# Optimization experiments

Measured on AMD Instinct MI355X. Metric: run time of the kernel, lower is better.

The kernel has to match this reference:

```python
import jax, jax.numpy as jnp
import numpy as np

B, L, E = 4, 1024, 1024
H = 16
HD = E // H
CLIP = 16
SCALE = 1.0 / np.sqrt(HD)


def setup_inputs() -> dict:
    key = jax.random.key(0)
    ks = jax.random.split(key, 13)
    def lin(k, fan_in, fan_out, gain):
        # xavier_uniform
        limit = gain * np.sqrt(6.0 / (fan_in + fan_out))
        return jax.random.uniform(k, (fan_out, fan_in), jnp.float32, -limit, limit)
    inv_sqrt2 = 1.0 / np.sqrt(2.0)
    return {
        "query": jax.random.normal(ks[0], (B, L, E), jnp.float32),
        "key": jax.random.normal(ks[1], (B, L, E), jnp.float32),
        "value": jax.random.normal(ks[2], (B, L, E), jnp.float32),
        "wq": lin(ks[3], E, E, inv_sqrt2), "bq": jnp.zeros((E,), jnp.float32),
        "wk": lin(ks[4], E, E, inv_sqrt2), "bk": jnp.zeros((E,), jnp.float32),
        "wv": lin(ks[5], E, E, inv_sqrt2), "bv": jnp.zeros((E,), jnp.float32),
        "wo": lin(ks[6], E, E, 1.0), "bo": jnp.zeros((E,), jnp.float32),
        "rel_k": jax.random.normal(ks[7], (2 * CLIP + 1, HD), jnp.float32) * 0.02,
        "rel_v": jax.random.normal(ks[8], (2 * CLIP + 1, HD), jnp.float32) * 0.02,
    }


def _heads(x):  # (B, L, E) -> (B, H, L, HD)
    return x.reshape(B, L, H, HD).transpose(0, 2, 1, 3)


def reference(query, key, value, wq, bq, wk, bk, wv, bv, wo, bo, rel_k, rel_v):
    q = _heads(query @ wq.T + bq)
    k = _heads(key @ wk.T + bk)
    v = _heads(value @ wv.T + bv)

    # relative-position index matrix (L_q, L_k), clipped to [-CLIP, CLIP]
    pos = jnp.arange(L)
    dist = jnp.clip(pos[None, :] - pos[:, None], -CLIP, CLIP) + CLIP
    r_k = rel_k[dist]  # (L, L, HD)
    r_v = rel_v[dist]  # (L, L, HD)

    dot = jnp.einsum('bhid,bhjd->bhij', q, k)
    rel = jnp.einsum('bhid,ijd->bhij', q, r_k)
    scores = (dot + rel) * SCALE
    attn = jax.nn.softmax(scores, axis=-1)

    y = jnp.einsum('bhij,bhjd->bhid', attn, v) + jnp.einsum('bhij,ijd->bhid', attn, r_v)
    y = y.transpose(0, 2, 1, 3).reshape(B, L, E)
    return y @ wo.T + bo
```

## Files before the change

kernel.cpp:

```cpp
#include <hip/hip_runtime.h>

#define BB 4
#define LL 1024
#define EE 1024
#define HH 16
#define HD 64
#define NBUCKET 33
#define SCALE 0.125f
#define SC2 (0.125f * 1.44269504088896f)

typedef unsigned short u16;
using f32x4 = __attribute__((ext_vector_type(4))) float;
using s16x8 = __attribute__((ext_vector_type(8))) short;

__device__ __forceinline__ u16 f2bf(float f) {
  union { float f; unsigned u; } x; x.f = f;
  unsigned r = (x.u + 0x7fffu + ((x.u >> 16) & 1u)) >> 16;
  return (u16)r;
}

__device__ __forceinline__ void gld_lds16(const void* g, void* s) {
  __builtin_amdgcn_global_load_lds((const __attribute__((address_space(1))) void*)g,
                                   (__attribute__((address_space(3))) void*)s, 16, 0, 0);
}

__device__ __forceinline__ float qsum16(float s) {
  s += __shfl_xor(s, 1); s += __shfl_xor(s, 2);
  s += __shfl_xor(s, 4); s += __shfl_xor(s, 8);
  return s;
}

__global__ __launch_bounds__(256) void cvt3_bf16(const float* __restrict__ a,
                                                 const float* __restrict__ b,
                                                 const float* __restrict__ c,
                                                 u16* __restrict__ oa, u16* __restrict__ ob,
                                                 u16* __restrict__ oc, int n4) {
  const int z = blockIdx.y;
  const float* in = z == 0 ? a : (z == 1 ? b : c);
  u16* out = z == 0 ? oa : (z == 1 ? ob : oc);
  int i = blockIdx.x * 256 + threadIdx.x;
  if (i < n4) {
    float4 f = ((const float4*)in)[i];
    ushort4 o;
    o.x = f2bf(f.x); o.y = f2bf(f.y); o.z = f2bf(f.z); o.w = f2bf(f.w);
    ((ushort4*)out)[i] = o;
  }
}

__global__ __launch_bounds__(256) void cvt4r_bf16(const float* __restrict__ a,
                                                  const float* __restrict__ b,
                                                  const float* __restrict__ c,
                                                  const float* __restrict__ d,
                                                  const float* __restrict__ rk,
                                                  u16* __restrict__ oa, u16* __restrict__ ob,
                                                  u16* __restrict__ oc, u16* __restrict__ od,
                                                  u16* __restrict__ ork, int n4) {
  const int z = blockIdx.z;
  int i = blockIdx.x * 256 + threadIdx.x;
  if (z == 4) {
    if (i < 48 * 64) ork[i] = (i < 33 * 64) ? f2bf(rk[i]) : (u16)0;
    return;
  }
  const float* in = z == 0 ? a : (z == 1 ? b : (z == 2 ? c : d));
  u16* out = z == 0 ? oa : (z == 1 ? ob : (z == 2 ? oc : od));
  if (i < n4) {
    float4 f = ((const float4*)in)[i];
    ushort4 o;
    o.x = f2bf(f.x); o.y = f2bf(f.y); o.z = f2bf(f.z); o.w = f2bf(f.w);
    ((ushort4*)out)[i] = o;
  }
}

template <int MODE>
__device__ __forceinline__ void gemm128_bt(const u16* __restrict__ A,
                                           const u16* __restrict__ Bw,
                                           const float* __restrict__ bias,
                                           u16* __restrict__ obf,
                                           float* __restrict__ ofp,
                                           int M, int N, int K, int m0, int n0) {
  __shared__ u16 a_sm[128 * 64];
  __shared__ u16 b_sm[128 * 64];
  const int tid = threadIdx.x;
  const int wave = tid >> 6, lane = tid & 63;
  const int row16 = lane & 15, quad = lane >> 4;
  const int wr = (wave >> 1) * 64, wc = (wave & 1) * 64;
  const int srow = lane >> 3, scol = (lane & 7) * 8;

  f32x4 acc[4][4] = {};

  for (int k0 = 0; k0 < K; k0 += 64) {
#pragma unroll
    for (int t = 0; t < 4; ++t) {
      const int chunk = wave * 4 + t;
      const int r = chunk * 8 + srow;
      gld_lds16(A + (size_t)(m0 + r) * K + k0 + scol, a_sm + chunk * 512);
      gld_lds16(Bw + (size_t)(n0 + r) * K + k0 + scol, b_sm + chunk * 512);
    }
    __syncthreads();
#pragma unroll
    for (int ks = 0; ks < 2; ++ks) {
      s16x8 af[4], bf[4];
#pragma unroll
      for (int mi = 0; mi < 4; ++mi)
        af[mi] = *(const s16x8*)&a_sm[(wr + mi * 16 + row16) * 64 + ks * 32 + quad * 8];
#pragma unroll
      for (int ni = 0; ni < 4; ++ni)
        bf[ni] = *(const s16x8*)&b_sm[(wc + ni * 16 + row16) * 64 + ks * 32 + quad * 8];
#pragma unroll
      for (int mi = 0; mi < 4; ++mi)
#pragma unroll
        for (int ni = 0; ni < 4; ++ni)
          acc[mi][ni] = __builtin_amdgcn_mfma_f32_16x16x32_bf16(af[mi], bf[ni], acc[mi][ni], 0, 0, 0);
    }
    __syncthreads();
  }

#pragma unroll
  for (int mi = 0; mi < 4; ++mi)
#pragma unroll
    for (int ni = 0; ni < 4; ++ni) {
      const int n = n0 + wc + ni * 16 + row16;
      const float bn = bias[n];
      if (MODE == 2) {
        const int mr0 = m0 + wr + mi * 16 + quad * 4;
        const int b = mr0 >> 10, l = mr0 & 1023;
        const int h = n >> 6, hd = n & 63;
        ushort4 o;
        o.x = f2bf(acc[mi][ni][0] + bn);
        o.y = f2bf(acc[mi][ni][1] + bn);
        o.z = f2bf(acc[mi][ni][2] + bn);
        o.w = f2bf(acc[mi][ni][3] + bn);
        *(ushort4*)&obf[((size_t)((b * HH + h) * HD + hd)) * LL + l] = o;
      } else {
#pragma unroll
        for (int r = 0; r < 4; ++r) {
          const int m = m0 + wr + mi * 16 + quad * 4 + r;
          const float v = acc[mi][ni][r] + bn;
          if (MODE == 0) {
            const int b = m >> 10, l = m & 1023, h = n >> 6, hd = n & 63;
            obf[((size_t)((b * HH + h) * LL + l)) * HD + hd] = f2bf(v);
          } else {
            ofp[(size_t)m * N + n] = v;
          }
        }
      }
    }
}

__global__ __launch_bounds__(256) void proj_gemm(
    const u16* __restrict__ xq, const u16* __restrict__ xk, const u16* __restrict__ xv,
    const u16* __restrict__ wqb, const u16* __restrict__ wkb, const u16* __restrict__ wvb,
    const float* __restrict__ bq, const float* __restrict__ bk, const float* __restrict__ bv,
    u16* __restrict__ oq, u16* __restrict__ ok, u16* __restrict__ ovt) {
  if (blockIdx.z == 0)
    gemm128_bt<0>(xq, wqb, bq, oq, nullptr, BB * LL, EE, EE, blockIdx.y * 128, blockIdx.x * 128);
  else if (blockIdx.z == 1)
    gemm128_bt<0>(xk, wkb, bk, ok, nullptr, BB * LL, EE, EE, blockIdx.y * 128, blockIdx.x * 128);
  else
    gemm128_bt<2>(xv, wvb, bv, ovt, nullptr, BB * LL, EE, EE, blockIdx.y * 128, blockIdx.x * 128);
}

__global__ __launch_bounds__(256) void out_gemm(const u16* __restrict__ Y,
                                                const u16* __restrict__ wob,
                                                const float* __restrict__ bo,
                                                float* __restrict__ out) {
  gemm128_bt<1>(Y, wob, bo, nullptr, out, BB * LL, EE, EE, blockIdx.y * 128, blockIdx.x * 128);
}

__global__ __launch_bounds__(256) void attn_fused(
    const u16* __restrict__ Q, const u16* __restrict__ Kb, const u16* __restrict__ Vt,
    const u16* __restrict__ RKp, const float* __restrict__ RV, u16* __restrict__ Y) {
  __shared__ __align__(16) float qr_sm[4][16 * 36];
  __shared__ __align__(16) float s_sm[4][16 * 36];
  __shared__ __align__(16) unsigned char kv[17408];

  const int tid = threadIdx.x;
  const int wave = tid >> 6, lane = tid & 63;
  const int row16 = lane & 15, quad = lane >> 4;
  const int bh = blockIdx.x & 63;
  const int i0 = (blockIdx.x >> 6) * 64;
  const int wq0 = i0 + wave * 16;
  const u16* qp = Q + (size_t)bh * LL * HD;
  const char* kpB = (const char*)(Kb + (size_t)bh * LL * HD);
  const char* vpB = (const char*)(Vt + (size_t)bh * HD * LL);

  u16* p_w = (u16*)(kv + wave * (16 * 72 * 2));
  float* qr_w = &qr_sm[wave][0];
  float* s_w = &s_sm[wave][0];

  for (int t = lane; t < 16 * 36; t += 64) s_w[t] = 0.f;

  int srcK[2], srcV[2];
#pragma unroll
  for (int t = 0; t < 2; ++t) {
    const int cK = (wave * 2 + t) * 64 + lane;
    const int rw = cK >> 3;
    const int cb = ((cK * 16) & 127) ^ ((rw & 7) << 4);
    srcK[t] = rw * 128 + cb;
    srcV[t] = rw * 2048 + cb;
  }
  const int swz = (row16 & 7) << 4;

  s16x8 qf[2];
#pragma unroll
  for (int ks = 0; ks < 2; ++ks)
    qf[ks] = *(const s16x8*)(qp + (size_t)(wq0 + row16) * HD + ks * 32 + quad * 8);

  f32x4 a0, a2;
#pragma unroll
  for (int nt = 0; nt < 3; ++nt) {
    f32x4 a = {};
#pragma unroll
    for (int ks = 0; ks < 2; ++ks) {
      s16x8 bfr = *(const s16x8*)(RKp + (size_t)(nt * 16 + row16) * HD + ks * 32 + quad * 8);
      a = __builtin_amdgcn_mfma_f32_16x16x32_bf16(qf[ks], bfr, a, 0, 0, 0);
    }
    if (nt == 0) a0 = a;
    if (nt == 2) a2 = a;
    const int idx = nt * 16 + row16;
    if (idx < NBUCKET)
#pragma unroll
      for (int r = 0; r < 4; ++r) qr_w[(quad * 4 + r) * 36 + idx] = a[r];
  }
  float blo[4], bhi[4];
#pragma unroll
  for (int r = 0; r < 4; ++r) {
    blo[r] = __shfl(a0[r], lane & 48);
    bhi[r] = __shfl(a2[r], lane & 48);
  }

  f32x4 oacc[4] = {};
  float rsum[4] = {0.f, 0.f, 0.f, 0.f};
  float plos[4] = {0.f, 0.f, 0.f, 0.f};
  float phis[4] = {0.f, 0.f, 0.f, 0.f};
  int dbase[4];
#pragma unroll
  for (int nt = 0; nt < 4; ++nt) dbase[nt] = nt * 16 + row16 - quad * 4 - wq0;

  for (int jt = 0; jt < 16; ++jt) {
    const int j0 = jt * 64;

#pragma unroll
    for (int t = 0; t < 2; ++t) {
      gld_lds16(kpB + (size_t)j0 * 128 + srcK[t], kv + (wave * 2 + t) * 1024);
      gld_lds16(vpB + (size_t)j0 * 2 + srcV[t], kv + 9216 + (wave * 2 + t) * 1024);
    }
    __syncthreads();

    f32x4 sacc[4] = {};
#pragma unroll
    for (int ks = 0; ks < 2; ++ks)
#pragma unroll
      for (int nt2 = 0; nt2 < 4; ++nt2) {
        const int L = (nt2 * 16 + row16) * 128 + ks * 64 + quad * 16;
        const s16x8 kfr = *(const s16x8*)(kv + (L ^ swz));
        sacc[nt2] = __builtin_amdgcn_mfma_f32_16x16x32_bf16(qf[ks], kfr, sacc[nt2], 0, 0, 0);
      }
    __syncthreads();

    float p[4][4];
    const bool far_lo = (wq0 >= j0 + 79);
    const bool far_hi = (j0 >= wq0 + 31);
    if (far_lo || far_hi) {
#pragma unroll
      for (int r = 0; r < 4; ++r) {
        const float bias = far_lo ? blo[r] : bhi[r];
        float acc = 0.f;
#pragma unroll
        for (int nt2 = 0; nt2 < 4; ++nt2) {
          const float pv = exp2f((sacc[nt2][r] + bias) * SC2);
          p[nt2][r] = pv;
          acc += pv;
        }
        rsum[r] += acc;
        if (far_lo) plos[r] += acc; else phis[r] += acc;
      }
    } else {
#pragma unroll
      for (int nt2 = 0; nt2 < 4; ++nt2)
#pragma unroll
        for (int r = 0; r < 4; ++r) {
          const int dr = dbase[nt2] + j0 - r;
          int bk = dr < -16 ? -16 : (dr > 16 ? 16 : dr);
          bk += 16;
          const float bias = qr_w[(quad * 4 + r) * 36 + bk];
          const float pv = exp2f((sacc[nt2][r] + bias) * SC2);
          p[nt2][r] = pv;
          rsum[r] += pv;
          if (dr <= -16) plos[r] += pv;
          else if (dr >= 16) phis[r] += pv;
          else atomicAdd(&s_w[(quad * 4 + r) * 36 + bk], pv);
        }
    }

#pragma unroll
    for (int nt2 = 0; nt2 < 4; ++nt2)
#pragma unroll
      for (int r = 0; r < 4; ++r)
        p_w[(quad * 4 + r) * 72 + nt2 * 16 + row16] = f2bf(p[nt2][r]);

#pragma unroll
    for (int ks = 0; ks < 2; ++ks) {
      const s16x8 pf = *(const s16x8*)&p_w[row16 * 72 + ks * 32 + quad * 8];
#pragma unroll
      for (int dt = 0; dt < 4; ++dt) {
        const int L = (dt * 16 + row16) * 128 + ks * 64 + quad * 16;
        const s16x8 vfr = *(const s16x8*)(kv + 9216 + (L ^ swz));
        oacc[dt] = __builtin_amdgcn_mfma_f32_16x16x32_bf16(pf, vfr, oacc[dt], 0, 0, 0);
      }
    }
    __syncthreads();
  }

  float lacc[4], slo[4], shi[4];
#pragma unroll
  for (int r = 0; r < 4; ++r) {
    lacc[r] = qsum16(rsum[r]);
    slo[r] = qsum16(plos[r]);
    shi[r] = qsum16(phis[r]);
  }

  __syncthreads();
  float* rv_sm = (float*)kv;
  for (int t = tid; t < NBUCKET * HD; t += 256) rv_sm[t] = RV[t];
  __syncthreads();

  const int b = bh >> 4, h = bh & 15;
#pragma unroll
  for (int r = 0; r < 4; ++r) {
    const int i_loc = quad * 4 + r;
    float rel[4] = {0.f, 0.f, 0.f, 0.f};
    for (int bk = 0; bk < NBUCKET; ++bk) {
      float sv = s_w[i_loc * 36 + bk];
      if (bk == 0) sv += slo[r];
      if (bk == 32) sv += shi[r];
#pragma unroll
      for (int dt = 0; dt < 4; ++dt) rel[dt] += sv * rv_sm[bk * HD + dt * 16 + row16];
    }
    const float inv = 1.0f / lacc[r];
#pragma unroll
    for (int dt = 0; dt < 4; ++dt) {
      const float y = (oacc[dt][r] + rel[dt]) * inv;
      Y[((size_t)(b * LL + wq0 + i_loc)) * EE + h * HD + dt * 16 + row16] = f2bf(y);
    }
  }
}

extern "C" void kernel_launch(void* const* d_in, const int* in_sizes, int n_in,
                              void* d_out, int out_size, void* d_ws, size_t ws_size,
                              hipStream_t stream) {
  const float* query = (const float*)d_in[0];
  const float* key_  = (const float*)d_in[1];
  const float* value = (const float*)d_in[2];
  const float* wq = (const float*)d_in[3];
  const float* bq = (const float*)d_in[4];
  const float* wk = (const float*)d_in[5];
  const float* bk = (const float*)d_in[6];
  const float* wv = (const float*)d_in[7];
  const float* bv = (const float*)d_in[8];
  const float* wo = (const float*)d_in[9];
  const float* bo = (const float*)d_in[10];
  const float* rel_k = (const float*)d_in[11];
  const float* rel_v = (const float*)d_in[12];

  char* base = (char*)d_ws;
  size_t off = 0;
  auto alloc = [&](size_t bytes) -> void* {
    void* p = base + off;
    off += (bytes + 255) & ~(size_t)255;
    return p;
  };
  const size_t XE = (size_t)BB * LL * EE;
  u16* xq    = (u16*)alloc(XE * 2);
  u16* xk    = (u16*)alloc(XE * 2);
  u16* xv    = (u16*)alloc(XE * 2);
  u16* wqb   = (u16*)alloc((size_t)EE * EE * 2);
  u16* wkb   = (u16*)alloc((size_t)EE * EE * 2);
  u16* wvb   = (u16*)alloc((size_t)EE * EE * 2);
  u16* wob   = (u16*)alloc((size_t)EE * EE * 2);
  u16* q_ws  = (u16*)alloc(XE * 2);
  u16* k_ws  = (u16*)alloc(XE * 2);
  u16* vt_ws = (u16*)alloc(XE * 2);
  u16* relkp = (u16*)alloc(48 * 64 * 2);
  u16* y_ws = xq;

  const int nx4 = (int)(XE / 4);
  const int nw4 = EE * EE / 4;
  cvt3_bf16<<<dim3(nx4 / 256, 3), 256, 0, stream>>>(query, key_, value, xq, xk, xv, nx4);
  cvt4r_bf16<<<dim3(nw4 / 256, 1, 5), 256, 0, stream>>>(wq, wk, wv, wo, rel_k,
                                                        wqb, wkb, wvb, wob, relkp, nw4);

  proj_gemm<<<dim3(EE / 128, BB * LL / 128, 3), 256, 0, stream>>>(
      xq, xk, xv, wqb, wkb, wvb, bq, bk, bv, q_ws, k_ws, vt_ws);

  attn_fused<<<1024, 256, 0, stream>>>(q_ws, k_ws, vt_ws, relkp, rel_v, y_ws);

  out_gemm<<<dim3(EE / 128, BB * LL / 128), 256, 0, stream>>>(y_ws, wob, bo, (float*)d_out);
}
```

Baseline: 279.3 us.

## Double-buffer K/V tiles in attention and merge conversion kernels into one launch

The attention kernel now uses two LDS buffers for K/V and prefetches the next 64-key tile while computing on the current one, so the global-to-LDS load no longer stalls each iteration. The per-iteration syncthreads are replaced by explicit waitcnt plus barrier, and P is packed to bf16 with v_cvt_pk_bf16_f32. The two fp32-to-bf16 conversion kernels are merged into a single launch. Doubling the K/V buffers raises LDS use per block, which may lower occupancy, and the P scratch now aliases the current K region, so correctness depends on the barrier placement.

```diff
diff --git a/kernel.cpp b/kernel.cpp
--- a/kernel.cpp
+++ b/kernel.cpp
@@ -30,44 +30,36 @@
   return s;
 }
 
-__global__ __launch_bounds__(256) void cvt3_bf16(const float* __restrict__ a,
-                                                 const float* __restrict__ b,
-                                                 const float* __restrict__ c,
-                                                 u16* __restrict__ oa, u16* __restrict__ ob,
-                                                 u16* __restrict__ oc, int n4) {
-  const int z = blockIdx.y;
-  const float* in = z == 0 ? a : (z == 1 ? b : c);
-  u16* out = z == 0 ? oa : (z == 1 ? ob : oc);
-  int i = blockIdx.x * 256 + threadIdx.x;
-  if (i < n4) {
+__global__ __launch_bounds__(256) void cvt_all(
+    const float* __restrict__ q, const float* __restrict__ k, const float* __restrict__ v,
+    const float* __restrict__ wq, const float* __restrict__ wk, const float* __restrict__ wv,
+    const float* __restrict__ wo, const float* __restrict__ rk,
+    u16* __restrict__ oq, u16* __restrict__ ok, u16* __restrict__ ov,
+    u16* __restrict__ owq, u16* __restrict__ owk, u16* __restrict__ owv,
+    u16* __restrict__ owo, u16* __restrict__ ork) {
+  const int bid = blockIdx.x;
+  const int tid = threadIdx.x;
+  if (bid < 12288) {
+    const int z = bid >> 12;
+    const int i = (bid & 4095) * 256 + tid;
+    const float* in = z == 0 ? q : (z == 1 ? k : v);
+    u16* out = z == 0 ? oq : (z == 1 ? ok : ov);
     float4 f = ((const float4*)in)[i];
     ushort4 o;
     o.x = f2bf(f.x); o.y = f2bf(f.y); o.z = f2bf(f.z); o.w = f2bf(f.w);
     ((ushort4*)out)[i] = o;
-  }
-}
-
-__global__ __launch_bounds__(256) void cvt4r_bf16(const float* __restrict__ a,
-                                                  const float* __restrict__ b,
-                                                  const float* __restrict__ c,
-                                                  const float* __restrict__ d,
-                                                  const float* __restrict__ rk,
-                                                  u16* __restrict__ oa, u16* __restrict__ ob,
-                                                  u16* __restrict__ oc, u16* __restrict__ od,
-                                                  u16* __restrict__ ork, int n4) {
-  const int z = blockIdx.z;
-  int i = blockIdx.x * 256 + threadIdx.x;
-  if (z == 4) {
-    if (i < 48 * 64) ork[i] = (i < 33 * 64) ? f2bf(rk[i]) : (u16)0;
-    return;
-  }
-  const float* in = z == 0 ? a : (z == 1 ? b : (z == 2 ? c : d));
-  u16* out = z == 0 ? oa : (z == 1 ? ob : (z == 2 ? oc : od));
-  if (i < n4) {
+  } else if (bid < 16384) {
+    const int z = (bid - 12288) >> 10;
+    const int i = ((bid - 12288) & 1023) * 256 + tid;
+    const float* in = z == 0 ? wq : (z == 1 ? wk : (z == 2 ? wv : wo));
+    u16* out = z == 0 ? owq : (z == 1 ? owk : (z == 2 ? owv : owo));
     float4 f = ((const float4*)in)[i];
     ushort4 o;
     o.x = f2bf(f.x); o.y = f2bf(f.y); o.z = f2bf(f.z); o.w = f2bf(f.w);
     ((ushort4*)out)[i] = o;
+  } else {
+    const int i = (bid - 16384) * 256 + tid;
+    ork[i] = (i < 33 * 64) ? f2bf(rk[i]) : (u16)0;
   }
 }
 
@@ -172,7 +164,7 @@
     const u16* __restrict__ RKp, const float* __restrict__ RV, u16* __restrict__ Y) {
   __shared__ __align__(16) float qr_sm[4][16 * 36];
   __shared__ __align__(16) float s_sm[4][16 * 36];
-  __shared__ __align__(16) unsigned char kv[17408];
+  __shared__ __align__(16) unsigned char kv[2][17408];
 
   const int tid = threadIdx.x;
   const int wave = tid >> 6, lane = tid & 63;
@@ -184,11 +176,8 @@
   const char* kpB = (const char*)(Kb + (size_t)bh * LL * HD);
   const char* vpB = (const char*)(Vt + (size_t)bh * HD * LL);
 
-  u16* p_w = (u16*)(kv + wave * (16 * 72 * 2));
   float* qr_w = &qr_sm[wave][0];
   float* s_w = &s_sm[wave][0];
-
-  for (int t = lane; t < 16 * 36; t += 64) s_w[t] = 0.f;
 
   int srcK[2], srcV[2];
 #pragma unroll
@@ -201,6 +190,14 @@
   }
   const int swz = (row16 & 7) << 4;
 
+#pragma unroll
+  for (int t = 0; t < 2; ++t) {
+    gld_lds16(kpB + srcK[t], kv[0] + (wave * 2 + t) * 1024);
+    gld_lds16(vpB + srcV[t], kv[0] + 9216 + (wave * 2 + t) * 1024);
+  }
+
+  for (int t = lane; t < 16 * 36; t += 64) s_w[t] = 0.f;
+
   s16x8 qf[2];
 #pragma unroll
   for (int ks = 0; ks < 2; ++ks)
@@ -237,15 +234,24 @@
 #pragma unroll
   for (int nt = 0; nt < 4; ++nt) dbase[nt] = nt * 16 + row16 - quad * 4 - wq0;
 
+  asm volatile("s_waitcnt vmcnt(0) lgkmcnt(0)" ::: "memory");
+  __builtin_amdgcn_s_barrier();
+  __builtin_amdgcn_sched_barrier(0);
+
   for (int jt = 0; jt < 16; ++jt) {
     const int j0 = jt * 64;
-
-#pragma unroll
-    for (int t = 0; t < 2; ++t) {
-      gld_lds16(kpB + (size_t)j0 * 128 + srcK[t], kv + (wave * 2 + t) * 1024);
-      gld_lds16(vpB + (size_t)j0 * 2 + srcV[t], kv + 9216 + (wave * 2 + t) * 1024);
-    }
-    __syncthreads();
+    unsigned char* kcur = (unsigned char*)kv[jt & 1];
+    unsigned char* knxt = (unsigned char*)kv[(jt & 1) ^ 1];
+    u16* p_w = (u16*)(kcur) + wave * 1152;
+
+    if (jt < 15) {
+      const size_t j1 = (size_t)(j0 + 64);
+#pragma unroll
+      for (int t = 0; t < 2; ++t) {
+        gld_lds16(kpB + j1 * 128 + srcK[t], knxt + (wave * 2 + t) * 1024);
+        gld_lds16(vpB + j1 * 2 + srcV[t], knxt + 9216 + (wave * 2 + t) * 1024);
+      }
+    }
 
     f32x4 sacc[4] = {};
 #pragma unroll
@@ -253,10 +259,12 @@
 #pragma unroll
       for (int nt2 = 0; nt2 < 4; ++nt2) {
         const int L = (nt2 * 16 + row16) * 128 + ks * 64 + quad * 16;
-        const s16x8 kfr = *(const s16x8*)(kv + (L ^ swz));
+        const s16x8 kfr = *(const s16x8*)(kcur + (L ^ swz));
         sacc[nt2] = __builtin_amdgcn_mfma_f32_16x16x32_bf16(qf[ks], kfr, sacc[nt2], 0, 0, 0);
       }
-    __syncthreads();
+    asm volatile("s_waitcnt lgkmcnt(0)" ::: "memory");
+    __builtin_amdgcn_s_barrier();
+    __builtin_amdgcn_sched_barrier(0);
 
     float p[4][4];
     const bool far_lo = (wq0 >= j0 + 79);
@@ -294,10 +302,17 @@
     }
 
 #pragma unroll
-    for (int nt2 = 0; nt2 < 4; ++nt2)
-#pragma unroll
-      for (int r = 0; r < 4; ++r)
-        p_w[(quad * 4 + r) * 72 + nt2 * 16 + row16] = f2bf(p[nt2][r]);
+    for (int nt2 = 0; nt2 < 4; ++nt2) {
+      const int c = nt2 * 16 + row16;
+#pragma unroll
+      for (int rr = 0; rr < 2; ++rr) {
+        unsigned pk;
+        asm("v_cvt_pk_bf16_f32 %0, %1, %2" : "=v"(pk)
+            : "v"(p[nt2][rr * 2]), "v"(p[nt2][rr * 2 + 1]));
+        p_w[(quad * 4 + rr * 2) * 72 + c] = (u16)pk;
+        p_w[(quad * 4 + rr * 2 + 1) * 72 + c] = (u16)(pk >> 16);
+      }
+    }
 
 #pragma unroll
     for (int ks = 0; ks < 2; ++ks) {
@@ -305,11 +320,14 @@
 #pragma unroll
       for (int dt = 0; dt < 4; ++dt) {
         const int L = (dt * 16 + row16) * 128 + ks * 64 + quad * 16;
-        const s16x8 vfr = *(const s16x8*)(kv + 9216 + (L ^ swz));
+        const s16x8 vfr = *(const s16x8*)(kcur + 9216 + (L ^ swz));
         oacc[dt] = __builtin_amdgcn_mfma_f32_16x16x32_bf16(pf, vfr, oacc[dt], 0, 0, 0);
       }
     }
-    __syncthreads();
+
+    asm volatile("s_waitcnt vmcnt(0) lgkmcnt(0)" ::: "memory");
+    __builtin_amdgcn_s_barrier();
+    __builtin_amdgcn_sched_barrier(0);
   }
 
   float lacc[4], slo[4], shi[4];
@@ -320,8 +338,7 @@
     shi[r] = qsum16(phis[r]);
   }
 
-  __syncthreads();
-  float* rv_sm = (float*)kv;
+  float* rv_sm = (float*)kv[0];
   for (int t = tid; t < NBUCKET * HD; t += 256) rv_sm[t] = RV[t];
   __syncthreads();
 
@@ -384,11 +401,8 @@
   u16* relkp = (u16*)alloc(48 * 64 * 2);
   u16* y_ws = xq;
 
-  const int nx4 = (int)(XE / 4);
-  const int nw4 = EE * EE / 4;
-  cvt3_bf16<<<dim3(nx4 / 256, 3), 256, 0, stream>>>(query, key_, value, xq, xk, xv, nx4);
-  cvt4r_bf16<<<dim3(nw4 / 256, 1, 5), 256, 0, stream>>>(wq, wk, wv, wo, rel_k,
-                                                        wqb, wkb, wvb, wob, relkp, nw4);
+  cvt_all<<<16396, 256, 0, stream>>>(query, key_, value, wq, wk, wv, wo, rel_k,
+                                     xq, xk, xv, wqb, wkb, wvb, wob, relkp);
 
   proj_gemm<<<dim3(EE / 128, BB * LL / 128, 3), 256, 0, stream>>>(
       xq, xk, xv, wqb, wkb, wvb, bq, bk, bv, q_ws, k_ws, vt_ws);
```

Result: no change. 278.8 us (-0.2%).
